# Kernel optimization log

Measured on AMD Instinct MI355X. Metric: run time of the kernel, lower is better.

The kernel has to match this reference:

```python
import jax, jax.numpy as jnp
import numpy as np

N_V, N_H, T, B = 1024, 512, 128, 256


def setup_inputs() -> dict:
    key = jax.random.key(0)
    k = jax.random.split(key, 3)
    v_data = (jax.random.uniform(k[0], (N_V, T, B)) < 0.5).astype(jnp.float32)  # binary visibles
    W = 0.01 * jax.random.normal(k[1], (N_H, N_V), jnp.float32)
    U = 0.01 * jax.random.normal(k[2], (N_H, N_H), jnp.float32)
    b_h = jnp.zeros((N_H,), jnp.float32)
    b_init = jnp.zeros((N_H,), jnp.float32)
    b_v = jnp.zeros((N_V,), jnp.float32)
    return {"v_data": v_data, "W": W, "U": U, "b_h": b_h, "b_init": b_init,
            "b_v": b_v, "CDk": 2}


def _sample_r_over_time(v, W, U, b_h, b_init):
    # v: (V,T,B) -> r: (H,T,B). Sequential mean-field recurrence over T
    # (RTRBM._sample_r_given_v_over_time: t=0 uses b_init and U=0, t>0 uses U,b_h).
    Wv = jnp.einsum('hv,vtb->thb', W, v)  # (T,H,B)
    r0 = jax.nn.sigmoid(Wv[0] + b_init[:, None])

    def step(r_lag, wv_t):
        r_t = jax.nn.sigmoid(wv_t + U @ r_lag + b_h[:, None])
        return r_t, r_t

    _, rs = jax.lax.scan(step, r0, Wv[1:])
    r = jnp.concatenate([r0[None], rs], axis=0)  # (T,H,B)
    return jnp.transpose(r, (1, 0, 2))  # (H,T,B)


def _parallel_r(v, r_lagged, W, U, b_h, b_init):
    # RTRBM._parallel_sample_r_h_given_v probabilities; v:(V,T,B), r_lagged:(H,T,B)
    r0 = jax.nn.sigmoid(jnp.einsum('hv,vb->hb', W, v[:, 0]) + b_init[:, None])
    rr = jax.nn.sigmoid(jnp.einsum('hv,vtb->htb', W, v[:, 1:])
                        + jnp.einsum('hr,rtb->htb', U, r_lagged[:, :-1])
                        + b_h[:, None, None])
    return jnp.concatenate([r0[:, None], rr], axis=1)  # (H,T,B)


def reference(v_data, W, U, b_h, b_init, b_v, CDk):
    key = jax.random.key(42)
    r_data = _sample_r_over_time(v_data, W, U, b_h, b_init)
    key, sk = jax.random.split(key)
    h_model = jax.random.bernoulli(sk, _parallel_r(v_data, r_data, W, U, b_h, b_init)).astype(v_data.dtype)
    for _ in range(CDk - 1):  # CD-k Gibbs chain (CDk is a concrete Python int)
        key, k1, k2 = jax.random.split(key, 3)
        v_prob = jax.nn.sigmoid(jnp.einsum('hv,htb->vtb', W, h_model) + b_v[:, None, None])
        v_model = jax.random.bernoulli(k1, v_prob).astype(v_data.dtype)
        h_model = jax.random.bernoulli(k2, _parallel_r(v_model, r_data, W, U, b_h, b_init)).astype(v_data.dtype)
    key, kf = jax.random.split(key)
    v_model = jax.random.bernoulli(
        kf, jax.nn.sigmoid(jnp.einsum('hv,htb->vtb', W, h_model) + b_v[:, None, None])
    ).astype(v_data.dtype)
    return (v_model, r_data)
```

## Files before the change

kernel.cpp:

```cpp
#include <hip/hip_runtime.h>
#include <stdint.h>

typedef unsigned long long u64;
typedef uint32_t u32;

#define NV 1024
#define NH 512
#define TT 128
#define BB 256
#define TBsz (TT*BB)
#define HTBsz (NH*TBsz)
#define VTBsz (NV*TBsz)
#define NWV (NV/64)
#define NWH (NH/64)
#define QCAP 1048576u
#define DELTA 5e-4
#define BTILE 2

__host__ __device__ inline void tf2x32(uint32_t k0, uint32_t k1,
                                       uint32_t x0, uint32_t x1,
                                       uint32_t& o0, uint32_t& o1) {
  const uint32_t ks2 = k0 ^ k1 ^ 0x1BD11BDAu;
#define ROTL(x,d) (((x)<<(d))|((x)>>(32-(d))))
#define RND(r) { x0 += x1; x1 = ROTL(x1,r); x1 ^= x0; }
  x0 += k0;  x1 += k1;
  RND(13) RND(15) RND(26) RND(6)
  x0 += k1;  x1 += ks2 + 1u;
  RND(17) RND(29) RND(16) RND(24)
  x0 += ks2; x1 += k0 + 2u;
  RND(13) RND(15) RND(26) RND(6)
  x0 += k0;  x1 += k1 + 3u;
  RND(17) RND(29) RND(16) RND(24)
  x0 += k1;  x1 += ks2 + 4u;
  RND(13) RND(15) RND(26) RND(6)
  x0 += ks2; x1 += k0 + 5u;
  o0 = x0; o1 = x1;
#undef RND
#undef ROTL
}

__device__ inline double tf_uniform64(uint32_t k0, uint32_t k1, uint32_t i) {
  uint32_t o0, o1;
  tf2x32(k0, k1, 0u, i, o0, o1);
  uint32_t bits = o0 ^ o1;
  uint32_t fb = (bits >> 9) | 0x3f800000u;
  float f = __uint_as_float(fb) - 1.0f;
  return (double)f;
}

__device__ inline double sigmoid64(double x) { return 1.0 / (1.0 + exp(-x)); }

__global__ __launch_bounds__(256) void kcvt(const float* __restrict__ s,
                                            double* __restrict__ d, int n) {
  int i = blockIdx.x * 256 + threadIdx.x;
  if (i < n) d[i] = (double)s[i];
}

__global__ __launch_bounds__(256) void kprepU(const float* __restrict__ U,
                                              float4* __restrict__ UB) {
  int i = blockIdx.x * 256 + threadIdx.x;
  int r4 = i / NH;
  int h  = i % NH;
  const float* __restrict__ p = U + (size_t)h*NH + r4*4;
  UB[i] = make_float4(p[0], p[1], p[2], p[3]);
}

__global__ __launch_bounds__(256) void kpack_f32(const float* __restrict__ in,
                                                 u64* __restrict__ out) {
  int tb = blockIdx.x * 256 + threadIdx.x;
  for (int w = 0; w < NWV; ++w) {
    u64 m = 0;
    #pragma unroll 8
    for (int j = 0; j < 64; ++j)
      m |= (u64)(in[(size_t)(w*64 + j)*TBsz + tb] != 0.0f ? 1 : 0) << j;
    out[(size_t)tb*NWV + w] = m;
  }
}

__global__ __launch_bounds__(256) void kWv(const u64* __restrict__ vb,
                                           const double* __restrict__ W64,
                                           double* __restrict__ WvT) {
  const int HM = 8;
  int t  = blockIdx.x / (NH/HM);
  int h0 = (blockIdx.x % (NH/HM)) * HM;
  int tb = t*BB + threadIdx.x;
  u64 m[NWV];
  #pragma unroll
  for (int w = 0; w < NWV; ++w) m[w] = vb[(size_t)tb*NWV + w];
  double acc[HM];
  #pragma unroll
  for (int i = 0; i < HM; ++i) acc[i] = 0.0;
  const double2* __restrict__ W2 = (const double2*)W64;
  for (int w = 0; w < NWV; ++w) {
    u64 mw = m[w];
    #pragma unroll 8
    for (int j2 = 0; j2 < 32; ++j2) {
      double bd0 = (double)((unsigned)((mw >> (2*j2+0)) & 1ull));
      double bd1 = (double)((unsigned)((mw >> (2*j2+1)) & 1ull));
      int vi = w*32 + j2;
      #pragma unroll
      for (int i = 0; i < HM; ++i) {
        double2 wv = W2[(size_t)(h0+i)*(NV/2) + vi];
        acc[i] = fma(bd0, wv.x, acc[i]);
        acc[i] = fma(bd1, wv.y, acc[i]);
      }
    }
  }
  #pragma unroll
  for (int i = 0; i < HM; ++i)
    WvT[(size_t)tb*NH + h0 + i] = acc[i];
}

__global__ __launch_bounds__(1024) void krecur(const double* __restrict__ WvT,
                                               const float4* __restrict__ UB,
                                               const float* __restrict__ bh,
                                               const float* __restrict__ binit,
                                               double* __restrict__ rT) {
  __shared__ double rA[BTILE][NH];
  const int b0 = blockIdx.x * BTILE;
  const int h = threadIdx.x & (NH-1);
  const int j = threadIdx.x >> 9;
  const double bhd = (double)bh[h];
  {
    double p = sigmoid64(WvT[(size_t)(b0+j)*NH + h] + (double)binit[h]);
    rA[j][h] = p;
    rT[(size_t)(b0+j)*NH + h] = p;
  }
  __syncthreads();
  for (int t = 1; t < TT; ++t) {
    double acc = WvT[((size_t)t*BB + b0 + j)*NH + h];
    double a0=0, a1=0, a2=0, a3=0;
    const double2* __restrict__ rA2 = (const double2*)rA[j];
    #pragma unroll 4
    for (int r = 0; r < NH; r += 4) {
      float4 u4 = UB[(size_t)(r >> 2)*NH + h];
      double2 q01 = rA2[(r>>1)+0];
      double2 q23 = rA2[(r>>1)+1];
      a0 = fma((double)u4.x, q01.x, a0);
      a1 = fma((double)u4.y, q01.y, a1);
      a2 = fma((double)u4.z, q23.x, a2);
      a3 = fma((double)u4.w, q23.y, a3);
    }
    __syncthreads();
    double p = sigmoid64((acc + ((a0+a1)+(a2+a3))) + bhd);
    rA[j][h] = p;
    rT[((size_t)t*BB + b0 + j)*NH + h] = p;
    __syncthreads();
  }
}

__global__ __launch_bounds__(256) void ktrans(const double* __restrict__ rT,
                                              float* __restrict__ out_r) {
  __shared__ double lds[32][33];
  int t  = blockIdx.x;
  int h0 = blockIdx.y * 32;
  int b0 = blockIdx.z * 32;
  int tx = threadIdx.x & 31;
  int ty = threadIdx.x >> 5;
  #pragma unroll
  for (int i = 0; i < 4; ++i) {
    int row = ty*4 + i;
    lds[row][tx] = rT[((size_t)t*BB + b0 + row)*NH + h0 + tx];
  }
  __syncthreads();
  #pragma unroll
  for (int i = 0; i < 4; ++i) {
    int row = ty*4 + i;
    out_r[(size_t)(h0+row)*TBsz + (size_t)t*BB + b0 + tx] = (float)lds[tx][row];
  }
}

__global__ __launch_bounds__(256) void ksample8(const double* __restrict__ rT,
                                                uint8_t* __restrict__ hbytes,
                                                u32 k0, u32 k1) {
  int i  = blockIdx.x * 256 + threadIdx.x;
  int tb = i >> 6;
  int hw = i & 63;
  int t = tb / BB, b = tb % BB;
  const double* __restrict__ rp = rT + ((size_t)t*BB + b)*NH + hw*8;
  unsigned byte = 0;
  #pragma unroll
  for (int j = 0; j < 8; ++j) {
    double p = rp[j];
    double u = tf_uniform64(k0, k1, (u32)((hw*8 + j)*TBsz + tb));
    byte |= (u < p) ? (1u << j) : 0u;
  }
  hbytes[(size_t)tb*(NH/8) + hw] = (uint8_t)byte;
}

__global__ __launch_bounds__(256) void kvis32(
    const float* __restrict__ W, const float* __restrict__ bv,
    const u64* __restrict__ hbits, uint8_t* __restrict__ vbytes,
    float* __restrict__ vf, u32* __restrict__ queue, u32* __restrict__ cnt,
    u32 k0, u32 k1) {
  const int VM = 8;
  int t  = blockIdx.x / (NV/VM);
  int v0 = (blockIdx.x % (NV/VM)) * VM;
  int tb = t*BB + threadIdx.x;
  u64 hb[NWH];
  #pragma unroll
  for (int w = 0; w < NWH; ++w) hb[w] = hbits[(size_t)tb*NWH + w];
  float acc[VM];
  #pragma unroll
  for (int i = 0; i < VM; ++i) acc[i] = 0.f;
  for (int w = 0; w < NWH; ++w) {
    u64 mw = hb[w];
    #pragma unroll 8
    for (int j = 0; j < 64; ++j) {
      float bd = (float)((u32)((mw >> j) & 1ull));
      const float* __restrict__ Wp = W + (size_t)(w*64 + j)*NV + v0;
      #pragma unroll
      for (int i = 0; i < VM; ++i) acc[i] = fmaf(bd, Wp[i], acc[i]);
    }
  }
  unsigned byte = 0;
  #pragma unroll
  for (int i = 0; i < VM; ++i) {
    float p = 1.f / (1.f + __expf(-(acc[i] + bv[v0+i])));
    size_t o = (size_t)(v0+i)*TBsz + tb;
    double u = tf_uniform64(k0, k1, (u32)o);
    double diff = (double)p - u;
    unsigned smp = diff > 0.0 ? 1u : 0u;
    if (fabs(diff) < DELTA) {
      u32 s = atomicAdd(cnt, 1u);
      if (s < QCAP) queue[s] = (u32)o;
    }
    byte |= smp << i;
    if (vf) vf[o] = (float)smp;
  }
  if (vbytes) vbytes[(size_t)tb*(NV/8) + (v0 >> 3)] = (uint8_t)byte;
}

__global__ __launch_bounds__(256) void kvis_fix(
    const float* __restrict__ W, const float* __restrict__ bv,
    const u64* __restrict__ hbits, u64* __restrict__ fixbits,
    float* __restrict__ vf, const u32* __restrict__ queue,
    const u32* __restrict__ cnt, u32 k0, u32 k1) {
  u32 n = *cnt; if (n > QCAP) n = QCAP;
  for (u32 q = blockIdx.x*256 + threadIdx.x; q < n; q += gridDim.x*256) {
    u32 o = queue[q];
    u32 v = o / TBsz, tb = o % TBsz;
    double a0=0, a1=0, a2=0, a3=0;
    for (int w = 0; w < NWH; ++w) {
      u64 mw = hbits[(size_t)tb*NWH + w];
      for (int j = 0; j < 64; j += 4) {
        if ((mw >> (j+0)) & 1ull) a0 += (double)W[(size_t)(w*64+j+0)*NV + v];
        if ((mw >> (j+1)) & 1ull) a1 += (double)W[(size_t)(w*64+j+1)*NV + v];
        if ((mw >> (j+2)) & 1ull) a2 += (double)W[(size_t)(w*64+j+2)*NV + v];
        if ((mw >> (j+3)) & 1ull) a3 += (double)W[(size_t)(w*64+j+3)*NV + v];
      }
    }
    double p = sigmoid64(((a0+a1)+(a2+a3)) + (double)bv[v]);
    double u = tf_uniform64(k0, k1, o);
    unsigned smp = (u < p) ? 1u : 0u;
    if (vf) vf[o] = (float)smp;
    if (fixbits) {
      size_t wi = (size_t)tb*NWV + (v >> 6);
      unsigned bit = v & 63u;
      unsigned cur = (unsigned)((fixbits[wi] >> bit) & 1ull);
      if (cur != smp) atomicXor(&fixbits[wi], 1ull << bit);
    }
  }
}

__global__ __launch_bounds__(256) void khid32(
    const u64* __restrict__ vbits, const float* __restrict__ W,
    const float* __restrict__ U, const float* __restrict__ bh,
    const float* __restrict__ binit, const float* __restrict__ r32,
    uint8_t* __restrict__ hbytes, u32* __restrict__ queue,
    u32* __restrict__ cnt, u32 k0, u32 k1) {
  const int HM = 8;
  int t  = blockIdx.x / (NH/HM);
  int h0 = (blockIdx.x % (NH/HM)) * HM;
  int tb = t*BB + threadIdx.x;
  u64 m[NWV];
  #pragma unroll
  for (int w = 0; w < NWV; ++w) m[w] = vbits[(size_t)tb*NWV + w];
  float acc[HM];
  #pragma unroll
  for (int i = 0; i < HM; ++i) acc[i] = 0.f;
  const float4* __restrict__ W4 = (const float4*)W;
  for (int w = 0; w < NWV; ++w) {
    u64 mw = m[w];
    #pragma unroll 4
    for (int j4 = 0; j4 < 16; ++j4) {
      float bd0 = (float)((u32)((mw >> (4*j4+0)) & 1ull));
      float bd1 = (float)((u32)((mw >> (4*j4+1)) & 1ull));
      float bd2 = (float)((u32)((mw >> (4*j4+2)) & 1ull));
      float bd3 = (float)((u32)((mw >> (4*j4+3)) & 1ull));
      int vi = w*16 + j4;
      #pragma unroll
      for (int i = 0; i < HM; ++i) {
        float4 wv = W4[(size_t)(h0+i)*(NV/4) + vi];
        acc[i] = fmaf(bd0, wv.x, acc[i]);
        acc[i] = fmaf(bd1, wv.y, acc[i]);
        acc[i] = fmaf(bd2, wv.z, acc[i]);
        acc[i] = fmaf(bd3, wv.w, acc[i]);
      }
    }
  }
  if (t > 0) {
    const float* __restrict__ rp = r32 + (size_t)(t-1)*BB + threadIdx.x;
    #pragma unroll 4
    for (int r = 0; r < NH; ++r) {
      float rv = rp[(size_t)r*TBsz];
      #pragma unroll
      for (int i = 0; i < HM; ++i)
        acc[i] = fmaf(U[(size_t)(h0+i)*NH + r], rv, acc[i]);
    }
    #pragma unroll
    for (int i = 0; i < HM; ++i) acc[i] += bh[h0+i];
  } else {
    #pragma unroll
    for (int i = 0; i < HM; ++i) acc[i] += binit[h0+i];
  }
  unsigned byte = 0;
  #pragma unroll
  for (int i = 0; i < HM; ++i) {
    float p = 1.f / (1.f + __expf(-acc[i]));
    size_t o = (size_t)(h0+i)*TBsz + tb;
    double u = tf_uniform64(k0, k1, (u32)o);
    double diff = (double)p - u;
    unsigned smp = diff > 0.0 ? 1u : 0u;
    if (fabs(diff) < DELTA) {
      u32 s = atomicAdd(cnt, 1u);
      if (s < QCAP) queue[s] = (u32)o;
    }
    byte |= smp << i;
  }
  hbytes[(size_t)tb*(NH/8) + (h0 >> 3)] = (uint8_t)byte;
}

__global__ __launch_bounds__(256) void khid_fix(
    const u64* __restrict__ vbits, const float* __restrict__ W,
    const double* __restrict__ U64, const float* __restrict__ bh,
    const float* __restrict__ binit, const double* __restrict__ rT,
    u64* __restrict__ fixbits, const u32* __restrict__ queue,
    const u32* __restrict__ cnt, u32 k0, u32 k1) {
  u32 n = *cnt; if (n > QCAP) n = QCAP;
  for (u32 q = blockIdx.x*256 + threadIdx.x; q < n; q += gridDim.x*256) {
    u32 o = queue[q];
    u32 h = o / TBsz, tb = o % TBsz;
    u32 t = tb / BB, b = tb % BB;
    double a0=0, a1=0, a2=0, a3=0;
    for (int w = 0; w < NWV; ++w) {
      u64 mw = vbits[(size_t)tb*NWV + w];
      for (int j = 0; j < 64; j += 4) {
        if ((mw >> (j+0)) & 1ull) a0 += (double)W[(size_t)h*NV + w*64+j+0];
        if ((mw >> (j+1)) & 1ull) a1 += (double)W[(size_t)h*NV + w*64+j+1];
        if ((mw >> (j+2)) & 1ull) a2 += (double)W[(size_t)h*NV + w*64+j+2];
        if ((mw >> (j+3)) & 1ull) a3 += (double)W[(size_t)h*NV + w*64+j+3];
      }
    }
    double logit = (a0+a1) + (a2+a3);
    if (t > 0) {
      const double* __restrict__ rp = rT + ((size_t)(t-1)*BB + b)*NH;
      const double* __restrict__ Ur = U64 + (size_t)h*NH;
      double u0=0, u1=0, u2=0, u3=0;
      for (int r = 0; r < NH; r += 4) {
        u0 = fma(Ur[r+0], rp[r+0], u0);
        u1 = fma(Ur[r+1], rp[r+1], u1);
        u2 = fma(Ur[r+2], rp[r+2], u2);
        u3 = fma(Ur[r+3], rp[r+3], u3);
      }
      logit = (logit + ((u0+u1)+(u2+u3))) + (double)bh[h];
    } else {
      logit += (double)binit[h];
    }
    double p = sigmoid64(logit);
    double u = tf_uniform64(k0, k1, o);
    unsigned smp = (u < p) ? 1u : 0u;
    size_t wi = (size_t)tb*NWH + (h >> 6);
    unsigned bit = h & 63u;
    unsigned cur = (unsigned)((fixbits[wi] >> bit) & 1ull);
    if (cur != smp) atomicXor(&fixbits[wi], 1ull << bit);
  }
}

extern "C" void kernel_launch(void* const* d_in, const int* in_sizes, int n_in,
                              void* d_out, int out_size, void* d_ws, size_t ws_size,
                              hipStream_t stream) {
  const float* vd    = (const float*)d_in[0];
  const float* W     = (const float*)d_in[1];
  const float* U     = (const float*)d_in[2];
  const float* bh    = (const float*)d_in[3];
  const float* binit = (const float*)d_in[4];
  const float* bv    = (const float*)d_in[5];

  float* out_v = (float*)d_out;
  float* out_r = (float*)d_out + VTBsz;
  double* WvT = (double*)d_out;

  char* w = (char*)d_ws;
  double* rT    = (double*)w;  w += (size_t)HTBsz*8;
  u64* vdbits   = (u64*)w;     w += (size_t)TBsz*NWV*8;
  u64* v1bits   = (u64*)w;     w += (size_t)TBsz*NWV*8;
  u64* h1bits   = (u64*)w;     w += (size_t)TBsz*NWH*8;
  u64* h2bits   = (u64*)w;     w += (size_t)TBsz*NWH*8;
  double* W64   = (double*)w;  w += (size_t)NH*NV*8;
  double* U64   = (double*)w;  w += (size_t)NH*NH*8;
  float4* UB    = (float4*)w;  w += (size_t)NH*NH*4;
  u32* q0       = (u32*)w;     w += (size_t)QCAP*4;
  u32* q1       = (u32*)w;     w += (size_t)QCAP*4;
  u32* q2       = (u32*)w;     w += (size_t)QCAP*4;
  u32* cnt      = (u32*)w;     w += 256;
  (void)ws_size; (void)in_sizes; (void)n_in; (void)out_size;

  uint32_t ka0,ka1, sk0,sk1;
  tf2x32(0u,42u, 0u,0u, ka0,ka1);
  tf2x32(0u,42u, 0u,1u, sk0,sk1);
  uint32_t kb0,kb1, k10,k11, k20,k21;
  tf2x32(ka0,ka1, 0u,0u, kb0,kb1);
  tf2x32(ka0,ka1, 0u,1u, k10,k11);
  tf2x32(ka0,ka1, 0u,2u, k20,k21);
  uint32_t kc0,kc1, kf0,kf1;
  tf2x32(kb0,kb1, 0u,0u, kc0,kc1);
  tf2x32(kb0,kb1, 0u,1u, kf0,kf1);

  hipMemsetAsync(cnt, 0, 3*sizeof(u32), stream);

  kcvt<<<(NH*NV+255)/256, 256, 0, stream>>>(W, W64, NH*NV);
  kcvt<<<(NH*NH+255)/256, 256, 0, stream>>>(U, U64, NH*NH);
  kprepU<<<(NH*NH/4)/256, 256, 0, stream>>>(U, UB);
  kpack_f32<<<TBsz/256, 256, 0, stream>>>(vd, vdbits);

  kWv<<<TT*(NH/8), 256, 0, stream>>>(vdbits, W64, WvT);

  krecur<<<BB/BTILE, NH*BTILE, 0, stream>>>(WvT, UB, bh, binit, rT);

  ktrans<<<dim3(TT, NH/32, BB/32), 256, 0, stream>>>(rT, out_r);

  ksample8<<<(TBsz*64)/256, 256, 0, stream>>>(rT, (uint8_t*)h1bits, sk0, sk1);

  kvis32<<<TT*(NV/8), 256, 0, stream>>>(W, bv, h1bits, (uint8_t*)v1bits, nullptr,
                                        q0, cnt+0, k10, k11);
  kvis_fix<<<128, 256, 0, stream>>>(W, bv, h1bits, v1bits, nullptr,
                                    q0, cnt+0, k10, k11);

  khid32<<<TT*(NH/8), 256, 0, stream>>>(v1bits, W, U, bh, binit, out_r,
                                        (uint8_t*)h2bits, q1, cnt+1, k20, k21);
  khid_fix<<<128, 256, 0, stream>>>(v1bits, W, U64, bh, binit, rT,
                                    h2bits, q1, cnt+1, k20, k21);

  kvis32<<<TT*(NV/8), 256, 0, stream>>>(W, bv, h2bits, nullptr, out_v,
                                        q2, cnt+2, kf0, kf1);
  kvis_fix<<<128, 256, 0, stream>>>(W, bv, h2bits, nullptr, out_v,
                                    q2, cnt+2, kf0, kf1);
}
```

Baseline: 5.869 ms.

## Double-buffer recurrence state, widen visible tiles, and transpose U for vector loads

The recurrence kernel now runs one batch column per 512-thread block and ping-pongs its LDS state buffer, so each time step needs one barrier instead of two. The visible kernel computes 16 outputs per thread with float4 loads of W and writes 16-bit packed results. The hidden kernel reads a pre-transposed copy of U with float4 loads instead of strided scalar loads. The costs are an extra transpose pass, more registers per thread in the visible kernel, and a halved block size in the recurrence, which reloads U once per batch column instead of once per pair of columns.

After: 4.982 ms. 15.1% less time.

```diff
diff --git a/kernel.cpp b/kernel.cpp
--- a/kernel.cpp
+++ b/kernel.cpp
@@ -15,7 +15,6 @@
 #define NWH (NH/64)
 #define QCAP 1048576u
 #define DELTA 5e-4
-#define BTILE 2
 
 __host__ __device__ inline void tf2x32(uint32_t k0, uint32_t k1,
                                        uint32_t x0, uint32_t x1,
@@ -65,6 +64,14 @@
   UB[i] = make_float4(p[0], p[1], p[2], p[3]);
 }
 
+__global__ __launch_bounds__(256) void kprepUT(const float* __restrict__ U,
+                                               float* __restrict__ UT) {
+  int i = blockIdx.x * 256 + threadIdx.x;
+  int r = i / NH;
+  int h = i % NH;
+  UT[i] = U[(size_t)h*NH + r];
+}
+
 __global__ __launch_bounds__(256) void kpack_f32(const float* __restrict__ in,
                                                  u64* __restrict__ out) {
   int tb = blockIdx.x * 256 + threadIdx.x;
@@ -111,26 +118,24 @@
     WvT[(size_t)tb*NH + h0 + i] = acc[i];
 }
 
-__global__ __launch_bounds__(1024) void krecur(const double* __restrict__ WvT,
-                                               const float4* __restrict__ UB,
-                                               const float* __restrict__ bh,
-                                               const float* __restrict__ binit,
-                                               double* __restrict__ rT) {
-  __shared__ double rA[BTILE][NH];
-  const int b0 = blockIdx.x * BTILE;
-  const int h = threadIdx.x & (NH-1);
-  const int j = threadIdx.x >> 9;
+__global__ __launch_bounds__(512) void krecur(const double* __restrict__ WvT,
+                                              const float4* __restrict__ UB,
+                                              const float* __restrict__ bh,
+                                              const float* __restrict__ binit,
+                                              double* __restrict__ rT) {
+  __shared__ double rA[2][NH];
+  const int b = blockIdx.x;
+  const int h = threadIdx.x;
   const double bhd = (double)bh[h];
-  {
-    double p = sigmoid64(WvT[(size_t)(b0+j)*NH + h] + (double)binit[h]);
-    rA[j][h] = p;
-    rT[(size_t)(b0+j)*NH + h] = p;
-  }
+  double p = sigmoid64(WvT[(size_t)b*NH + h] + (double)binit[h]);
+  rA[0][h] = p;
+  rT[(size_t)b*NH + h] = p;
   __syncthreads();
+  int cur = 0;
   for (int t = 1; t < TT; ++t) {
-    double acc = WvT[((size_t)t*BB + b0 + j)*NH + h];
+    double acc = WvT[((size_t)t*BB + b)*NH + h];
     double a0=0, a1=0, a2=0, a3=0;
-    const double2* __restrict__ rA2 = (const double2*)rA[j];
+    const double2* __restrict__ rA2 = (const double2*)rA[cur];
     #pragma unroll 4
     for (int r = 0; r < NH; r += 4) {
       float4 u4 = UB[(size_t)(r >> 2)*NH + h];
@@ -141,11 +146,11 @@
       a2 = fma((double)u4.z, q23.x, a2);
       a3 = fma((double)u4.w, q23.y, a3);
     }
+    p = sigmoid64((acc + ((a0+a1)+(a2+a3))) + bhd);
+    rA[cur ^ 1][h] = p;
+    rT[((size_t)t*BB + b)*NH + h] = p;
     __syncthreads();
-    double p = sigmoid64((acc + ((a0+a1)+(a2+a3))) + bhd);
-    rA[j][h] = p;
-    rT[((size_t)t*BB + b0 + j)*NH + h] = p;
-    __syncthreads();
+    cur ^= 1;
   }
 }
 
@@ -193,7 +198,7 @@
     const u64* __restrict__ hbits, uint8_t* __restrict__ vbytes,
     float* __restrict__ vf, u32* __restrict__ queue, u32* __restrict__ cnt,
     u32 k0, u32 k1) {
-  const int VM = 8;
+  const int VM = 16;
   int t  = blockIdx.x / (NV/VM);
   int v0 = (blockIdx.x % (NV/VM)) * VM;
   int tb = t*BB + threadIdx.x;
@@ -205,15 +210,31 @@
   for (int i = 0; i < VM; ++i) acc[i] = 0.f;
   for (int w = 0; w < NWH; ++w) {
     u64 mw = hb[w];
-    #pragma unroll 8
+    #pragma unroll 4
     for (int j = 0; j < 64; ++j) {
       float bd = (float)((u32)((mw >> j) & 1ull));
-      const float* __restrict__ Wp = W + (size_t)(w*64 + j)*NV + v0;
-      #pragma unroll
-      for (int i = 0; i < VM; ++i) acc[i] = fmaf(bd, Wp[i], acc[i]);
-    }
-  }
-  unsigned byte = 0;
+      const float4* __restrict__ Wp4 =
+          (const float4*)(W + (size_t)(w*64 + j)*NV + v0);
+      float4 w0 = Wp4[0], w1 = Wp4[1], w2 = Wp4[2], w3 = Wp4[3];
+      acc[ 0] = fmaf(bd, w0.x, acc[ 0]);
+      acc[ 1] = fmaf(bd, w0.y, acc[ 1]);
+      acc[ 2] = fmaf(bd, w0.z, acc[ 2]);
+      acc[ 3] = fmaf(bd, w0.w, acc[ 3]);
+      acc[ 4] = fmaf(bd, w1.x, acc[ 4]);
+      acc[ 5] = fmaf(bd, w1.y, acc[ 5]);
+      acc[ 6] = fmaf(bd, w1.z, acc[ 6]);
+      acc[ 7] = fmaf(bd, w1.w, acc[ 7]);
+      acc[ 8] = fmaf(bd, w2.x, acc[ 8]);
+      acc[ 9] = fmaf(bd, w2.y, acc[ 9]);
+      acc[10] = fmaf(bd, w2.z, acc[10]);
+      acc[11] = fmaf(bd, w2.w, acc[11]);
+      acc[12] = fmaf(bd, w3.x, acc[12]);
+      acc[13] = fmaf(bd, w3.y, acc[13]);
+      acc[14] = fmaf(bd, w3.z, acc[14]);
+      acc[15] = fmaf(bd, w3.w, acc[15]);
+    }
+  }
+  unsigned bits = 0;
   #pragma unroll
   for (int i = 0; i < VM; ++i) {
     float p = 1.f / (1.f + __expf(-(acc[i] + bv[v0+i])));
@@ -225,10 +246,11 @@
       u32 s = atomicAdd(cnt, 1u);
       if (s < QCAP) queue[s] = (u32)o;
     }
-    byte |= smp << i;
+    bits |= smp << i;
     if (vf) vf[o] = (float)smp;
   }
-  if (vbytes) vbytes[(size_t)tb*(NV/8) + (v0 >> 3)] = (uint8_t)byte;
+  if (vbytes)
+    *(uint16_t*)(vbytes + (size_t)tb*(NV/8) + (v0 >> 3)) = (uint16_t)bits;
 }
 
 __global__ __launch_bounds__(256) void kvis_fix(
@@ -265,7 +287,7 @@
 
 __global__ __launch_bounds__(256) void khid32(
     const u64* __restrict__ vbits, const float* __restrict__ W,
-    const float* __restrict__ U, const float* __restrict__ bh,
+    const float* __restrict__ UT, const float* __restrict__ bh,
     const float* __restrict__ binit, const float* __restrict__ r32,
     uint8_t* __restrict__ hbytes, u32* __restrict__ queue,
     u32* __restrict__ cnt, u32 k0, u32 k1) {
@@ -301,12 +323,20 @@
   }
   if (t > 0) {
     const float* __restrict__ rp = r32 + (size_t)(t-1)*BB + threadIdx.x;
+    const float4* __restrict__ UT4 = (const float4*)UT;
     #pragma unroll 4
     for (int r = 0; r < NH; ++r) {
       float rv = rp[(size_t)r*TBsz];
-      #pragma unroll
-      for (int i = 0; i < HM; ++i)
-        acc[i] = fmaf(U[(size_t)(h0+i)*NH + r], rv, acc[i]);
+      float4 ua = UT4[(size_t)r*(NH/4) + (h0 >> 2) + 0];
+      float4 ub = UT4[(size_t)r*(NH/4) + (h0 >> 2) + 1];
+      acc[0] = fmaf(ua.x, rv, acc[0]);
+      acc[1] = fmaf(ua.y, rv, acc[1]);
+      acc[2] = fmaf(ua.z, rv, acc[2]);
+      acc[3] = fmaf(ua.w, rv, acc[3]);
+      acc[4] = fmaf(ub.x, rv, acc[4]);
+      acc[5] = fmaf(ub.y, rv, acc[5]);
+      acc[6] = fmaf(ub.z, rv, acc[6]);
+      acc[7] = fmaf(ub.w, rv, acc[7]);
     }
     #pragma unroll
     for (int i = 0; i < HM; ++i) acc[i] += bh[h0+i];
@@ -400,6 +430,7 @@
   double* W64   = (double*)w;  w += (size_t)NH*NV*8;
   double* U64   = (double*)w;  w += (size_t)NH*NH*8;
   float4* UB    = (float4*)w;  w += (size_t)NH*NH*4;
+  float* UT     = (float*)w;   w += (size_t)NH*NH*4;
   u32* q0       = (u32*)w;     w += (size_t)QCAP*4;
   u32* q1       = (u32*)w;     w += (size_t)QCAP*4;
   u32* q2       = (u32*)w;     w += (size_t)QCAP*4;
@@ -422,28 +453,29 @@
   kcvt<<<(NH*NV+255)/256, 256, 0, stream>>>(W, W64, NH*NV);
   kcvt<<<(NH*NH+255)/256, 256, 0, stream>>>(U, U64, NH*NH);
   kprepU<<<(NH*NH/4)/256, 256, 0, stream>>>(U, UB);
+  kprepUT<<<(NH*NH)/256, 256, 0, stream>>>(U, UT);
   kpack_f32<<<TBsz/256, 256, 0, stream>>>(vd, vdbits);
 
   kWv<<<TT*(NH/8), 256, 0, stream>>>(vdbits, W64, WvT);
 
-  krecur<<<BB/BTILE, NH*BTILE, 0, stream>>>(WvT, UB, bh, binit, rT);
+  krecur<<<BB, NH, 0, stream>>>(WvT, UB, bh, binit, rT);
 
   ktrans<<<dim3(TT, NH/32, BB/32), 256, 0, stream>>>(rT, out_r);
 
   ksample8<<<(TBsz*64)/256, 256, 0, stream>>>(rT, (uint8_t*)h1bits, sk0, sk1);
 
-  kvis32<<<TT*(NV/8), 256, 0, stream>>>(W, bv, h1bits, (uint8_t*)v1bits, nullptr,
-                                        q0, cnt+0, k10, k11);
+  kvis32<<<TT*(NV/16), 256, 0, stream>>>(W, bv, h1bits, (uint8_t*)v1bits, nullptr,
+                                         q0, cnt+0, k10, k11);
   kvis_fix<<<128, 256, 0, stream>>>(W, bv, h1bits, v1bits, nullptr,
                                     q0, cnt+0, k10, k11);
 
-  khid32<<<TT*(NH/8), 256, 0, stream>>>(v1bits, W, U, bh, binit, out_r,
+  khid32<<<TT*(NH/8), 256, 0, stream>>>(v1bits, W, UT, bh, binit, out_r,
                                         (uint8_t*)h2bits, q1, cnt+1, k20, k21);
   khid_fix<<<128, 256, 0, stream>>>(v1bits, W, U64, bh, binit, rT,
                                     h2bits, q1, cnt+1, k20, k21);
 
-  kvis32<<<TT*(NV/8), 256, 0, stream>>>(W, bv, h2bits, nullptr, out_v,
-                                        q2, cnt+2, kf0, kf1);
+  kvis32<<<TT*(NV/16), 256, 0, stream>>>(W, bv, h2bits, nullptr, out_v,
+                                         q2, cnt+2, kf0, kf1);
   kvis_fix<<<128, 256, 0, stream>>>(W, bv, h2bits, nullptr, out_v,
                                     q2, cnt+2, kf0, kf1);
 }
```
